# Kernel tuning notes

Measured on AMD Instinct MI355X. Metric: run time of the kernel, lower is better.

## Reference

```python
import jax, jax.numpy as jnp
import numpy as np

KERNEL_SIZE = 2
TEMPERATURE = 1.0
EPS = 1e-5


def _ln(y, g, b):
    mu = jnp.mean(y, axis=-1, keepdims=True)
    var = jnp.mean((y - mu) ** 2, axis=-1, keepdims=True)
    return g * (y - mu) * jax.lax.rsqrt(var + EPS) + b


def _window_sum_before(h, k):
    # sum of h shifted right by 1..k (zero padded), matching get_hidden_states_before
    B, L, H = h.shape
    out = jnp.zeros_like(h)
    for s in range(1, k + 1):
        out = out + jnp.pad(h, ((0, 0), (s, 0), (0, 0)))[:, :L, :]
    return out


def _window_sum_after(h, k):
    B, L, H = h.shape
    out = jnp.zeros_like(h)
    for s in range(1, k + 1):
        out = out + jnp.pad(h, ((0, 0), (0, s), (0, 0)))[:, s:, :]
    return out


def setup_inputs():
    H, B, L = 512, 8, 1024
    std = 0.1
    key = jax.random.key(0)
    ks = jax.random.split(key, 12)
    return {
        "word_inputs": jax.random.normal(ks[0], (B, L, H), jnp.float32),
        "mask": jnp.zeros((B, L), jnp.float32),  # 1 = padding
        "num_layers": 3,
        "Wg": std * jax.random.normal(ks[1], (4 * H, 8 * H), jnp.float32),
        "bg": std * jax.random.normal(ks[2], (8 * H,), jnp.float32),
        "Wemb": std * jax.random.normal(ks[3], (H, 8 * H), jnp.float32),
        "Wdg": std * jax.random.normal(ks[4], (2 * H, 2 * H), jnp.float32),
        "bdg": std * jax.random.normal(ks[5], (2 * H,), jnp.float32),
        "Wdf": std * jax.random.normal(ks[6], (2 * H, H), jnp.float32),
        "bdf": std * jax.random.normal(ks[7], (H,), jnp.float32),
        "Wet": std * jax.random.normal(ks[8], (H, H), jnp.float32),
        "bet": jnp.zeros((H,), jnp.float32),
        "W1": std * jax.random.normal(ks[9], (H, 2 * H), jnp.float32),
        "b1": jnp.zeros((2 * H,), jnp.float32),
        "W2": std * jax.random.normal(ks[10], (2 * H, H), jnp.float32),
        "b2": jnp.zeros((H,), jnp.float32),
        "ln_g": jnp.ones((11, H), jnp.float32),   # order: i,o,l,f1,f2,f3,f4,gd,go,gf,h
        "ln_b": jnp.zeros((11, H), jnp.float32),
    }


def reference(word_inputs, mask, num_layers, Wg, bg, Wemb, Wdg, bdg, Wdf, bdf,
              Wet, bet, W1, b1, W2, b2, ln_g, ln_b):
    B, L, H = word_inputs.shape
    seq_mask = (1.0 - mask)[:, :, None]          # (B,L,1), 1 = real token
    softmax_neg = (-mask * 1e25)[:, :, None]     # (B,L,1)
    lens = jnp.sum(seq_mask, axis=1)             # (B,1)

    x = word_inputs * seq_mask
    h, c = x, x
    dh = jnp.sum(h, axis=1) / lens               # (B,H) dummy/sentence node
    dc = jnp.sum(c, axis=1) / lens

    we_cat = x @ Wemb                            # (B,L,8H) embedding gate terms
    emb_tr = jnp.tanh(x @ Wet + bet)             # (B,L,H)

    # dummy-gate weight chunks, mirroring torch chunk/split layout
    gWxd, gWhd = Wdg[:H, :H], Wdg[H:, :H]
    gWxo, gWho = Wdg[:H, H:], Wdg[H:, H:]
    gbd, gbo = bdg[:H], bdg[H:]
    gWxf, gWhf = Wdf[:H], Wdf[H:]

    for _ in range(num_layers):
        hb = _window_sum_before(h, KERNEL_SIZE) * seq_mask
        ha = _window_sum_after(h, KERNEL_SIZE) * seq_mask
        cb = _window_sum_before(c, KERNEL_SIZE) * seq_mask
        ca = _window_sum_after(c, KERNEL_SIZE) * seq_mask
        d_in = jnp.broadcast_to(dh[:, None, :], (B, L, H))

        # single fused 4H -> 8H gate GEMM plus precomputed embedding gates
        gates = jnp.concatenate([h, hb, ha, d_in], axis=-1) @ Wg + bg + we_cat
        fl, fr, fc_, fd, gi, ge, gw, go = jnp.split(gates, 8, axis=-1)

        g_fl = jax.nn.sigmoid(_ln(fl, ln_g[3], ln_b[3]))
        g_fr = jax.nn.sigmoid(_ln(fr, ln_g[4], ln_b[4]))
        g_fc = jax.nn.sigmoid(_ln(fc_, ln_g[5], ln_b[5]))
        g_fd = jax.nn.sigmoid(_ln(fd, ln_g[6], ln_b[6]))
        g_i = jax.nn.sigmoid(_ln(gi, ln_g[0], ln_b[0]))
        g_e = jax.nn.sigmoid(_ln(ge, ln_g[2], ln_b[2]))
        g_o = jax.nn.sigmoid(_ln(go, ln_g[1], ln_b[1]))
        cand = jnp.tanh(gw)

        # normalize the five write sources across gates (S-LSTM softmax combination)
        five = jax.nn.softmax(
            jnp.stack([g_fl, g_fr, g_fc, g_fd, g_i], axis=0) / TEMPERATURE, axis=0)
        c_new = (five[0] * cb + five[1] * ca + five[2] * c
                 + five[3] * dc[:, None, :] + five[4] * cand)
        h_new = g_o * jnp.tanh(c_new) + g_e * emb_tr

        h = h_new * seq_mask
        c = c_new * seq_mask

        # dummy (sentence-level) node update with position softmax attention
        avg_h = jnp.sum(h, axis=1) / lens
        g_d = jax.nn.sigmoid(_ln(dh @ gWxd + avg_h @ gWhd + gbd, ln_g[7], ln_b[7]))
        g_do = jax.nn.sigmoid(_ln(dh @ gWxo + avg_h @ gWho + gbo, ln_g[8], ln_b[8]))
        g_f = jax.nn.sigmoid(_ln((dh @ gWxf)[:, None, :] + h @ gWhf + bdf,
                                 ln_g[9], ln_b[9]))          # (B,L,H)
        scores = jax.nn.softmax(
            jnp.concatenate([g_f + softmax_neg, g_d[:, None, :]], axis=1)
            / TEMPERATURE, axis=1)                            # (B,L+1,H)
        dc = jnp.sum(scores[:, :L] * c, axis=1) + scores[:, L] * dc
        dh = g_do * jnp.tanh(dc)

    # position-wise FFN + residual + final LayerNorm (dropout off / eval mode)
    out = h + (jnp.maximum(h @ W1 + b1, 0.0) @ W2 + b2)
    out = _ln(out, ln_g[10], ln_b[10])
    return out * seq_mask
```

## Files before the change

### kernel.cpp

```cpp
#include <hip/hip_runtime.h>
#include <hip/hip_bf16.h>

typedef __hip_bfloat16 bf16;
typedef __attribute__((ext_vector_type(8))) short bf16x8;
typedef __attribute__((ext_vector_type(4))) float f32x4;

#define B_ 8
#define L_ 1024
#define H_ 512
#define BL_ (B_ * L_)
#define BLH_ ((size_t)BL_ * H_)
#define NCH 32
#define CHL (L_ / NCH)
#define NLAYERS 3

__device__ __forceinline__ float b2f(bf16 x) { return __bfloat162float(x); }
__device__ __forceinline__ bf16  f2b(float x) { return __float2bfloat16(x); }
__device__ __forceinline__ short f2bs(float x) { bf16 h = f2b(x); return *(short*)&h; }
__device__ __forceinline__ float bsf(short s) {
    union { unsigned int i; float f; } u; u.i = ((unsigned int)(unsigned short)s) << 16; return u.f;
}
__device__ __forceinline__ float sigm(float x) { return 1.f / (1.f + expf(-x)); }

__device__ __forceinline__ void gload16(const void* g, void* l) {
    __builtin_amdgcn_global_load_lds((const __attribute__((address_space(1))) void*)g,
                                     (__attribute__((address_space(3))) void*)l, 16, 0, 0);
}


__global__ __launch_bounds__(256) void cvtT_k(const float* __restrict__ src, bf16* __restrict__ dst,
                                              int R, int C, int ldD, int co) {
    __shared__ float t[32][33];
    int tx = threadIdx.x & 31, ty = threadIdx.x >> 5;
    int c = blockIdx.x * 32 + tx;
    int rb = blockIdx.y * 32;
    #pragma unroll
    for (int i = 0; i < 4; ++i)
        t[ty + i * 8][tx] = src[(size_t)(rb + ty + i * 8) * C + c];
    __syncthreads();
    #pragma unroll
    for (int i = 0; i < 4; ++i)
        dst[(size_t)(blockIdx.x * 32 + ty + i * 8) * ldD + co + rb + tx] = f2b(t[tx][ty + i * 8]);
}

__global__ __launch_bounds__(256) void init_k(const float* __restrict__ word, const float* __restrict__ mask,
                                              bf16* __restrict__ xbf, bf16* __restrict__ h0, bf16* __restrict__ c0,
                                              bf16* __restrict__ A) {
    size_t idx = (size_t)blockIdx.x * 256 + threadIdx.x;
    if (idx >= BLH_) return;
    int bl = (int)(idx >> 9);
    int hh = (int)(idx & 511);
    float sm = 1.f - mask[bl];
    bf16 w = f2b(word[idx] * sm);
    xbf[idx] = w; h0[idx] = w; c0[idx] = w;
    A[((size_t)bl << 11) + 1536 + hh] = w;
}

__global__ __launch_bounds__(256) void lens_k(const float* __restrict__ mask, float* __restrict__ lens) {
    __shared__ float sr[4];
    int b = blockIdx.x, t = threadIdx.x;
    float s = 0.f;
    for (int l = t; l < L_; l += 256) s += 1.f - mask[b * L_ + l];
    #pragma unroll
    for (int off = 32; off > 0; off >>= 1) s += __shfl_down(s, off);
    if ((t & 63) == 0) sr[t >> 6] = s;
    __syncthreads();
    if (t == 0) lens[b] = sr[0] + sr[1] + sr[2] + sr[3];
}

__global__ __launch_bounds__(512) void colsum_k(const bf16* __restrict__ src, float* __restrict__ partial) {
    int h = threadIdx.x, ch = blockIdx.x, b = blockIdx.y;
    float s = 0.f;
    #pragma unroll 4
    for (int i = 0; i < CHL; ++i)
        s += b2f(src[((size_t)(b * L_ + ch * CHL + i) << 9) + h]);
    partial[((size_t)(b * NCH + ch) << 9) + h] = s;
}

__global__ __launch_bounds__(512) void avgcomb_k(const float* __restrict__ partial, const float* __restrict__ lens,
                                                 float* __restrict__ o1, float* __restrict__ o2) {
    int h = threadIdx.x, b = blockIdx.x;
    float s = 0.f;
    #pragma unroll
    for (int ch = 0; ch < NCH; ++ch) s += partial[((size_t)(b * NCH + ch) << 9) + h];
    float a = s / lens[b];
    o1[(b << 9) + h] = a;
    if (o2) o2[(b << 9) + h] = a;
}


__global__ __launch_bounds__(256) void gemm_mfma_k(const bf16* __restrict__ A, const bf16* __restrict__ Bt,
                                                   const float* __restrict__ bias, const float* __restrict__ addB,
                                                   bf16* __restrict__ C, int M, int N, int K, int mode) {
    __shared__ __align__(16) bf16 As[2 * 128 * 32];
    __shared__ __align__(16) bf16 Bs[2 * 128 * 32];
    const int tid = threadIdx.x;
    const int lane = tid & 63, wv = tid >> 6;
    const int wm = wv >> 1, wn = wv & 1;
    const int m0 = blockIdx.y * 128, n0 = blockIdx.x * 128;

    const int r0 = tid >> 2, c0 = (tid & 3) * 8;
    const bf16* Ar0 = A + (size_t)(m0 + r0) * K + c0;
    const bf16* Ar1 = A + (size_t)(m0 + r0 + 64) * K + c0;
    const bf16* Br0 = Bt + (size_t)(n0 + r0) * K + c0;
    const bf16* Br1 = Bt + (size_t)(n0 + r0 + 64) * K + c0;
    bf16* lA0 = As + (size_t)tid * 8;
    bf16* lA1 = As + (size_t)(tid + 256) * 8;
    bf16* lB0 = Bs + (size_t)tid * 8;
    bf16* lB1 = Bs + (size_t)(tid + 256) * 8;

    f32x4 acc[4][4] = {};
    const int fr = lane & 15, fq = lane >> 4;
    const bf16* aP = As + (size_t)(wm * 64 + fr) * 32 + fq * 8;
    const bf16* bP = Bs + (size_t)(wn * 64 + fr) * 32 + fq * 8;

    for (int k0 = 0; k0 < K; k0 += 64) {
        #pragma unroll
        for (int h = 0; h < 2; ++h) {
            gload16(Ar0 + k0 + h * 32, lA0 + h * 4096);
            gload16(Ar1 + k0 + h * 32, lA1 + h * 4096);
            gload16(Br0 + k0 + h * 32, lB0 + h * 4096);
            gload16(Br1 + k0 + h * 32, lB1 + h * 4096);
        }
        __syncthreads();
        #pragma unroll
        for (int h = 0; h < 2; ++h) {
            bf16x8 af[4], bfr[4];
            #pragma unroll
            for (int i = 0; i < 4; ++i) {
                af[i]  = *(const bf16x8*)(aP + h * 4096 + (size_t)i * 16 * 32);
                bfr[i] = *(const bf16x8*)(bP + h * 4096 + (size_t)i * 16 * 32);
            }
            #pragma unroll
            for (int i = 0; i < 4; ++i)
                #pragma unroll
                for (int j = 0; j < 4; ++j)
                    acc[i][j] = __builtin_amdgcn_mfma_f32_16x16x32_bf16(af[i], bfr[j], acc[i][j], 0, 0, 0);
        }
        __syncthreads();
    }
    const float* abp = addB ? addB + (size_t)(m0 >> 10) * N : nullptr;
    #pragma unroll
    for (int j = 0; j < 4; ++j) {
        int n = n0 + wn * 64 + j * 16 + fr;
        float bb = bias ? bias[n] : 0.f;
        if (abp) bb += abp[n];
        #pragma unroll
        for (int i = 0; i < 4; ++i) {
            #pragma unroll
            for (int r = 0; r < 4; ++r) {
                int m = m0 + wm * 64 + i * 16 + fq * 4 + r;
                float v = acc[i][j][r] + bb;
                if (mode == 1) v = fmaxf(v, 0.f);
                else if (mode == 2) v = tanhf(v);
                C[(size_t)m * N + n] = f2b(v);
            }
        }
    }
}


#define PRE_BUILD_BLOCKS ((int)(BLH_ / 8 / 256))
__global__ __launch_bounds__(256) void pre_k(const bf16* __restrict__ h, const float* __restrict__ mask,
                                             bf16* __restrict__ A, const float* __restrict__ dh,
                                             const bf16* __restrict__ WdhT, const float* __restrict__ bg,
                                             float* __restrict__ dhG) {
    __shared__ float a[512];
    if (blockIdx.x >= PRE_BUILD_BLOCKS) {
        int e = blockIdx.x - PRE_BUILD_BLOCKS;
        int b = e >> 4, nb = e & 15;
        int t = threadIdx.x;
        a[t] = dh[(b << 9) + t];
        a[t + 256] = dh[(b << 9) + t + 256];
        __syncthreads();
        int n = nb * 256 + t;
        const bf16* wr = WdhT + (size_t)n * 512;
        float acc = bg[n];
        #pragma unroll 8
        for (int i = 0; i < 64; ++i) {
            bf16x8 w = *(const bf16x8*)(wr + i * 8);
            #pragma unroll
            for (int j = 0; j < 8; ++j) acc = fmaf(a[i * 8 + j], bsf(w[j]), acc);
        }
        dhG[(size_t)b * 4096 + n] = acc;
        return;
    }
    int i = blockIdx.x * 256 + threadIdx.x;
    int h8 = i & 63, bl = i >> 6;
    int l = bl & 1023;
    float sm = 1.f - mask[bl];
    size_t src = ((size_t)bl << 9) + (h8 << 3);
    bf16x8 hv = *(const bf16x8*)(h + src);
    float hb[8] = {}, ha[8] = {};
    if (l >= 1) { bf16x8 v = *(const bf16x8*)(h + src - 512);
        #pragma unroll
        for (int e = 0; e < 8; ++e) hb[e] += bsf(v[e]); }
    if (l >= 2) { bf16x8 v = *(const bf16x8*)(h + src - 1024);
        #pragma unroll
        for (int e = 0; e < 8; ++e) hb[e] += bsf(v[e]); }
    if (l <= L_ - 2) { bf16x8 v = *(const bf16x8*)(h + src + 512);
        #pragma unroll
        for (int e = 0; e < 8; ++e) ha[e] += bsf(v[e]); }
    if (l <= L_ - 3) { bf16x8 v = *(const bf16x8*)(h + src + 1024);
        #pragma unroll
        for (int e = 0; e < 8; ++e) ha[e] += bsf(v[e]); }
    bf16x8 hbv, hav;
    #pragma unroll
    for (int e = 0; e < 8; ++e) { hbv[e] = f2bs(hb[e] * sm); hav[e] = f2bs(ha[e] * sm); }
    size_t base = ((size_t)bl << 11) + (h8 << 3);
    *(bf16x8*)(A + base)        = hv;
    *(bf16x8*)(A + base + 512)  = hbv;
    *(bf16x8*)(A + base + 1024) = hav;
}

__global__ __launch_bounds__(256) void fuse_k(const bf16* __restrict__ gates,
                                              const float* __restrict__ lng, const float* __restrict__ lnb,
                                              const bf16* __restrict__ cin, const bf16* __restrict__ emb,
                                              const float* __restrict__ mask, const float* __restrict__ dc,
                                              bf16* __restrict__ hout, bf16* __restrict__ cout) {
    const int lane = threadIdx.x & 63;
    const int bl = (blockIdx.x << 2) + (threadIdx.x >> 6);
    const int l = bl & 1023, b = bl >> 10;
    const float sm = 1.f - mask[bl];
    const int e0 = lane << 3;
    const bf16* gp = gates + ((size_t)bl << 12) + e0;
    float g[8][8];
    #pragma unroll
    for (int j = 0; j < 8; ++j) {
        bf16x8 v = *(const bf16x8*)(gp + (j << 9));
        #pragma unroll
        for (int i = 0; i < 8; ++i) g[j][i] = bsf(v[i]);
    }
    const int js[7]  = {0, 1, 2, 3, 4, 5, 7};
    const int lis[7] = {3, 4, 5, 6, 0, 2, 1};
    #pragma unroll
    for (int jj = 0; jj < 7; ++jj) {
        const int j = js[jj];
        float s = 0.f, q = 0.f;
        #pragma unroll
        for (int i = 0; i < 8; ++i) { s += g[j][i]; q += g[j][i] * g[j][i]; }
        #pragma unroll
        for (int off = 32; off > 0; off >>= 1) { s += __shfl_xor(s, off); q += __shfl_xor(q, off); }
        float mu = s * (1.f / 512.f);
        float rs = rsqrtf(q * (1.f / 512.f) - mu * mu + 1e-5f);
        float gmv[8], btv[8];
        const float* gm = lng + lis[jj] * 512 + e0;
        const float* bt = lnb + lis[jj] * 512 + e0;
        *(float4*)&gmv[0] = *(const float4*)gm;       *(float4*)&gmv[4] = *(const float4*)(gm + 4);
        *(float4*)&btv[0] = *(const float4*)bt;       *(float4*)&btv[4] = *(const float4*)(bt + 4);
        #pragma unroll
        for (int i = 0; i < 8; ++i)
            g[j][i] = sigm(gmv[i] * (g[j][i] - mu) * rs + btv[i]);
    }
    size_t ci = ((size_t)bl << 9) + e0;
    float cm[8] = {}, cp[8] = {}, ccv[8], ev[8], dcv[8];
    {
        bf16x8 v = *(const bf16x8*)(cin + ci);
        #pragma unroll
        for (int i = 0; i < 8; ++i) ccv[i] = bsf(v[i]);
    }
    if (l >= 1) { bf16x8 v = *(const bf16x8*)(cin + ci - 512);
        #pragma unroll
        for (int i = 0; i < 8; ++i) cm[i] += bsf(v[i]); }
    if (l >= 2) { bf16x8 v = *(const bf16x8*)(cin + ci - 1024);
        #pragma unroll
        for (int i = 0; i < 8; ++i) cm[i] += bsf(v[i]); }
    if (l <= L_ - 2) { bf16x8 v = *(const bf16x8*)(cin + ci + 512);
        #pragma unroll
        for (int i = 0; i < 8; ++i) cp[i] += bsf(v[i]); }
    if (l <= L_ - 3) { bf16x8 v = *(const bf16x8*)(cin + ci + 1024);
        #pragma unroll
        for (int i = 0; i < 8; ++i) cp[i] += bsf(v[i]); }
    {
        bf16x8 v = *(const bf16x8*)(emb + ci);
        #pragma unroll
        for (int i = 0; i < 8; ++i) ev[i] = bsf(v[i]);
    }
    *(float4*)&dcv[0] = *(const float4*)(dc + (b << 9) + e0);
    *(float4*)&dcv[4] = *(const float4*)(dc + (b << 9) + e0 + 4);
    bf16x8 hv, cv;
    #pragma unroll
    for (int i = 0; i < 8; ++i) {
        float mx = fmaxf(fmaxf(fmaxf(g[0][i], g[1][i]), fmaxf(g[2][i], g[3][i])), g[4][i]);
        float w0 = expf(g[0][i] - mx), w1 = expf(g[1][i] - mx), w2 = expf(g[2][i] - mx);
        float w3 = expf(g[3][i] - mx), w4 = expf(g[4][i] - mx);
        float inv = 1.f / (w0 + w1 + w2 + w3 + w4);
        float cand = tanhf(g[6][i]);
        float cn = (w0 * cm[i] * sm + w1 * cp[i] * sm + w2 * ccv[i] + w3 * dcv[i] + w4 * cand) * inv;
        float hn = g[7][i] * tanhf(cn) + g[5][i] * ev[i];
        hv[i] = f2bs(hn * sm);
        cv[i] = f2bs(cn * sm);
    }
    *(bf16x8*)(hout + ci) = hv;
    *(bf16x8*)(cout + ci) = cv;
}

__global__ __launch_bounds__(512) void dgu_k(const float* __restrict__ dh, const float* __restrict__ partial,
                                             const float* __restrict__ lens,
                                             const bf16* __restrict__ WdgT, const float* __restrict__ bdg,
                                             const bf16* __restrict__ WdfT0, const float* __restrict__ bdf,
                                             const float* __restrict__ lng, const float* __restrict__ lnb,
                                             float* __restrict__ gd, float* __restrict__ gdo, float* __restrict__ u) {
    __shared__ float a2[1024];
    __shared__ float sred[16];
    int t = threadIdx.x, bx = blockIdx.x, b = blockIdx.y;
    a2[t] = dh[(b << 9) + t];
    {
        float s = 0.f;
        #pragma unroll
        for (int ch = 0; ch < NCH; ++ch) s += partial[((size_t)(b * NCH + ch) << 9) + t];
        a2[512 + t] = s / lens[b];
    }
    __syncthreads();
    if (bx == 2) {
        const bf16* wr = WdfT0 + (size_t)t * 512;
        float acc = bdf[t];
        #pragma unroll 8
        for (int i = 0; i < 64; ++i) {
            bf16x8 w = *(const bf16x8*)(wr + i * 8);
            #pragma unroll
            for (int j = 0; j < 8; ++j) acc = fmaf(a2[i * 8 + j], bsf(w[j]), acc);
        }
        u[(b << 9) + t] = acc;
        return;
    }
    int col = (bx << 9) + t;
    const bf16* wr = WdgT + (size_t)col * 1024;
    float acc = bdg[col];
    #pragma unroll 8
    for (int i = 0; i < 128; ++i) {
        bf16x8 w = *(const bf16x8*)(wr + i * 8);
        #pragma unroll
        for (int j = 0; j < 8; ++j) acc = fmaf(a2[i * 8 + j], bsf(w[j]), acc);
    }
    float s = acc, q = acc * acc;
    #pragma unroll
    for (int off = 32; off > 0; off >>= 1) { s += __shfl_down(s, off); q += __shfl_down(q, off); }
    int w = t >> 6;
    if ((t & 63) == 0) { sred[w] = s; sred[8 + w] = q; }
    __syncthreads();
    float S = 0.f, Q = 0.f;
    #pragma unroll
    for (int i = 0; i < 8; ++i) { S += sred[i]; Q += sred[8 + i]; }
    float mu = S * (1.f / 512.f);
    float var = Q * (1.f / 512.f) - mu * mu;
    int li = 7 + bx;
    float n = lng[li * 512 + t] * (acc - mu) * rsqrtf(var + 1e-5f) + lnb[li * 512 + t];
    float g = sigm(n);
    if (bx) gdo[(b << 9) + t] = g; else gd[(b << 9) + t] = g;
}

__global__ __launch_bounds__(256) void gfln_k(bf16* __restrict__ gf, const float* __restrict__ lng,
                                              const float* __restrict__ lnb) {
    const int lane = threadIdx.x & 63;
    const int bl = (blockIdx.x << 2) + (threadIdx.x >> 6);
    const int e0 = lane << 3;
    size_t ci = ((size_t)bl << 9) + e0;
    float v[8];
    {
        bf16x8 gv = *(const bf16x8*)(gf + ci);
        #pragma unroll
        for (int i = 0; i < 8; ++i) v[i] = bsf(gv[i]);
    }
    float s = 0.f, q = 0.f;
    #pragma unroll
    for (int i = 0; i < 8; ++i) { s += v[i]; q += v[i] * v[i]; }
    #pragma unroll
    for (int off = 32; off > 0; off >>= 1) { s += __shfl_xor(s, off); q += __shfl_xor(q, off); }
    float mu = s * (1.f / 512.f);
    float rs = rsqrtf(q * (1.f / 512.f) - mu * mu + 1e-5f);
    float gmv[8], btv[8];
    const float* gm = lng + 9 * 512 + e0;
    const float* bt = lnb + 9 * 512 + e0;
    *(float4*)&gmv[0] = *(const float4*)gm;  *(float4*)&gmv[4] = *(const float4*)(gm + 4);
    *(float4*)&btv[0] = *(const float4*)bt;  *(float4*)&btv[4] = *(const float4*)(bt + 4);
    bf16x8 ov;
    #pragma unroll
    for (int i = 0; i < 8; ++i) ov[i] = f2bs(sigm(gmv[i] * (v[i] - mu) * rs + btv[i]));
    *(bf16x8*)(gf + ci) = ov;
}

__global__ __launch_bounds__(512) void attnp_k(const bf16* __restrict__ gf, const float* __restrict__ mask,
                                               const bf16* __restrict__ cc, float* __restrict__ pm,
                                               float* __restrict__ ps, float* __restrict__ pa) {
    int h = threadIdx.x, ch = blockIdx.x, b = blockIdx.y;
    float m = -INFINITY, s = 0.f, acc = 0.f;
    for (int i = 0; i < CHL; ++i) {
        int l = ch * CHL + i;
        size_t idx = ((size_t)(b * L_ + l) << 9) + h;
        float v = b2f(gf[idx]) - mask[b * L_ + l] * 1e25f;
        float mn = fmaxf(m, v);
        float sc = expf(m - mn);
        float p = expf(v - mn);
        s = s * sc + p;
        acc = acc * sc + p * b2f(cc[idx]);
        m = mn;
    }
    size_t o = ((size_t)(b * NCH + ch) << 9) + h;
    pm[o] = m; ps[o] = s; pa[o] = acc;
}

__global__ __launch_bounds__(512) void attnc_k(const float* __restrict__ pm, const float* __restrict__ ps,
                                               const float* __restrict__ pa, const float* __restrict__ gd,
                                               const float* __restrict__ gdo, float* __restrict__ dc,
                                               float* __restrict__ dh) {
    int h = threadIdx.x, b = blockIdx.x;
    float M = -INFINITY, S = 0.f, A = 0.f;
    #pragma unroll
    for (int ch = 0; ch < NCH; ++ch) {
        size_t o = ((size_t)(b * NCH + ch) << 9) + h;
        float m = pm[o], s = ps[o], a = pa[o];
        float Mn = fmaxf(M, m);
        float e1 = expf(M - Mn), e2 = expf(m - Mn);
        S = S * e1 + s * e2;
        A = A * e1 + a * e2;
        M = Mn;
    }
    float v = gd[(b << 9) + h];
    float Mn = fmaxf(M, v);
    float e1 = expf(M - Mn), e2 = expf(v - Mn);
    float dcold = dc[(b << 9) + h];
    S = S * e1 + e2;
    A = A * e1 + e2 * dcold;
    float dcn = A / S;
    dc[(b << 9) + h] = dcn;
    dh[(b << 9) + h] = gdo[(b << 9) + h] * tanhf(dcn);
}

__global__ __launch_bounds__(256) void final_k(const bf16* __restrict__ hfin, const bf16* __restrict__ t2,
                                               const float* __restrict__ lng, const float* __restrict__ lnb,
                                               const float* __restrict__ mask, float* __restrict__ out) {
    const int lane = threadIdx.x & 63;
    const int bl = (blockIdx.x << 2) + (threadIdx.x >> 6);
    const int e0 = lane << 3;
    size_t ci = ((size_t)bl << 9) + e0;
    float v[8];
    {
        bf16x8 a = *(const bf16x8*)(hfin + ci);
        bf16x8 bb = *(const bf16x8*)(t2 + ci);
        #pragma unroll
        for (int i = 0; i < 8; ++i) v[i] = bsf(a[i]) + bsf(bb[i]);
    }
    float s = 0.f, q = 0.f;
    #pragma unroll
    for (int i = 0; i < 8; ++i) { s += v[i]; q += v[i] * v[i]; }
    #pragma unroll
    for (int off = 32; off > 0; off >>= 1) { s += __shfl_xor(s, off); q += __shfl_xor(q, off); }
    float mu = s * (1.f / 512.f);
    float rs = rsqrtf(q * (1.f / 512.f) - mu * mu + 1e-5f);
    float gmv[8], btv[8];
    const float* gm = lng + 10 * 512 + e0;
    const float* bt = lnb + 10 * 512 + e0;
    *(float4*)&gmv[0] = *(const float4*)gm;  *(float4*)&gmv[4] = *(const float4*)(gm + 4);
    *(float4*)&btv[0] = *(const float4*)bt;  *(float4*)&btv[4] = *(const float4*)(bt + 4);
    float sm = 1.f - mask[bl];
    float o[8];
    #pragma unroll
    for (int i = 0; i < 8; ++i) o[i] = (gmv[i] * (v[i] - mu) * rs + btv[i]) * sm;
    *(float4*)(out + ci)     = *(float4*)&o[0];
    *(float4*)(out + ci + 4) = *(float4*)&o[4];
}


extern "C" void kernel_launch(void* const* d_in, const int* in_sizes, int n_in,
                              void* d_out, int out_size, void* d_ws, size_t ws_size,
                              hipStream_t stream) {
    const float* word = (const float*)d_in[0];
    const float* mask = (const float*)d_in[1];
    const float* Wg   = (const float*)d_in[3];
    const float* bg   = (const float*)d_in[4];
    const float* Wemb = (const float*)d_in[5];
    const float* Wdg  = (const float*)d_in[6];
    const float* bdg  = (const float*)d_in[7];
    const float* Wdf  = (const float*)d_in[8];
    const float* bdf  = (const float*)d_in[9];
    const float* Wet  = (const float*)d_in[10];
    const float* bet  = (const float*)d_in[11];
    const float* W1   = (const float*)d_in[12];
    const float* b1   = (const float*)d_in[13];
    const float* W2   = (const float*)d_in[14];
    const float* b2   = (const float*)d_in[15];
    const float* lng  = (const float*)d_in[16];
    const float* lnb  = (const float*)d_in[17];
    float* out = (float*)d_out;

    char* base = (char*)d_ws;
    size_t off = 0;
    auto alloc = [&](size_t bytes) -> void* {
        void* r = base + off;
        off += (bytes + 255) & ~(size_t)255;
        return r;
    };
    bf16* h0    = (bf16*)alloc(BLH_ * 2);
    bf16* h1    = (bf16*)alloc(BLH_ * 2);
    bf16* c0    = (bf16*)alloc(BLH_ * 2);
    bf16* c1    = (bf16*)alloc(BLH_ * 2);
    bf16* xbf   = (bf16*)alloc(BLH_ * 2);
    bf16* emb   = (bf16*)alloc(BLH_ * 2);
    bf16* Abuf  = (bf16*)alloc((size_t)BL_ * 2048 * 2);
    bf16* gf    = (bf16*)alloc(BLH_ * 2);
    bf16* t1    = (bf16*)alloc((size_t)BL_ * 1024 * 2);
    bf16* t2    = (bf16*)alloc(BLH_ * 2);
    bf16* WcatT = (bf16*)alloc((size_t)4096 * 2048 * 2);
    bf16* gates = (bf16*)alloc((size_t)BL_ * 4096 * 2);
    bf16* WetT  = (bf16*)alloc((size_t)512 * 512 * 2);
    bf16* WhfT  = (bf16*)alloc((size_t)512 * 512 * 2);
    bf16* W1T   = (bf16*)alloc((size_t)1024 * 512 * 2);
    bf16* W2T   = (bf16*)alloc((size_t)512 * 1024 * 2);
    bf16* WdhT  = (bf16*)alloc((size_t)4096 * 512 * 2);
    bf16* WdgT  = (bf16*)alloc((size_t)1024 * 1024 * 2);
    bf16* WdfT0 = (bf16*)alloc((size_t)512 * 512 * 2);
    float* dhG  = (float*)alloc((size_t)B_ * 4096 * 4);
    float* pm   = (float*)alloc((size_t)B_ * NCH * H_ * 4);
    float* ps   = (float*)alloc((size_t)B_ * NCH * H_ * 4);
    float* pa   = (float*)alloc((size_t)B_ * NCH * H_ * 4);
    float* lens = (float*)alloc(B_ * 4);
    float* dh   = (float*)alloc(B_ * H_ * 4);
    float* dc   = (float*)alloc(B_ * H_ * 4);
    float* avgh = (float*)alloc(B_ * H_ * 4);
    float* gd   = (float*)alloc(B_ * H_ * 4);
    float* gdo  = (float*)alloc(B_ * H_ * 4);
    float* u    = (float*)alloc(B_ * H_ * 4);
    (void)ws_size; (void)in_sizes; (void)n_in; (void)out_size; (void)avgh;

    cvtT_k<<<dim3(128, 48), 256, 0, stream>>>(Wg,   WcatT, 1536, 4096, 2048, 0);
    cvtT_k<<<dim3(128, 16), 256, 0, stream>>>(Wemb, WcatT,  512, 4096, 2048, 1536);
    cvtT_k<<<dim3(16, 16),  256, 0, stream>>>(Wet,  WetT,   512,  512,  512, 0);
    cvtT_k<<<dim3(16, 16),  256, 0, stream>>>(Wdf + (size_t)512 * 512, WhfT, 512, 512, 512, 0);
    cvtT_k<<<dim3(32, 16),  256, 0, stream>>>(W1,   W1T,    512, 1024,  512, 0);
    cvtT_k<<<dim3(16, 32),  256, 0, stream>>>(W2,   W2T,   1024,  512, 1024, 0);
    cvtT_k<<<dim3(128, 16), 256, 0, stream>>>(Wg + (size_t)1536 * 4096, WdhT, 512, 4096, 512, 0);
    cvtT_k<<<dim3(32, 32),  256, 0, stream>>>(Wdg,  WdgT,  1024, 1024, 1024, 0);
    cvtT_k<<<dim3(16, 16),  256, 0, stream>>>(Wdf,  WdfT0,  512,  512,  512, 0);

    const int eb = (int)((BLH_ + 255) / 256);
    init_k<<<eb, 256, 0, stream>>>(word, mask, xbf, h0, c0, Abuf);
    lens_k<<<B_, 256, 0, stream>>>(mask, lens);
    colsum_k<<<dim3(NCH, B_), 512, 0, stream>>>(xbf, pm);
    avgcomb_k<<<B_, 512, 0, stream>>>(pm, lens, dh, dc);

    gemm_mfma_k<<<dim3(4, 64), 256, 0, stream>>>(xbf, WetT, bet, nullptr, emb, BL_, 512, 512, 2);

    bf16 *hcur = h0, *ccur = c0, *hnxt = h1, *cnxt = c1;
    for (int layer = 0; layer < NLAYERS; ++layer) {
        pre_k<<<PRE_BUILD_BLOCKS + 16 * B_, 256, 0, stream>>>(hcur, mask, Abuf, dh, WdhT, bg, dhG);
        gemm_mfma_k<<<dim3(32, 64), 256, 0, stream>>>(Abuf, WcatT, nullptr, dhG, gates, BL_, 4096, 2048, 0);
        fuse_k<<<BL_ / 4, 256, 0, stream>>>(gates, lng, lnb, ccur, emb, mask, dc, hnxt, cnxt);
        colsum_k<<<dim3(NCH, B_), 512, 0, stream>>>(hnxt, pm);
        dgu_k<<<dim3(3, B_), 512, 0, stream>>>(dh, pm, lens, WdgT, bdg, WdfT0, bdf, lng, lnb, gd, gdo, u);
        gemm_mfma_k<<<dim3(4, 64), 256, 0, stream>>>(hnxt, WhfT, nullptr, u, gf, BL_, 512, 512, 0);
        gfln_k<<<BL_ / 4, 256, 0, stream>>>(gf, lng, lnb);
        attnp_k<<<dim3(NCH, B_), 512, 0, stream>>>(gf, mask, cnxt, pm, ps, pa);
        attnc_k<<<B_, 512, 0, stream>>>(pm, ps, pa, gd, gdo, dc, dh);
        bf16* t;
        t = hcur; hcur = hnxt; hnxt = t;
        t = ccur; ccur = cnxt; cnxt = t;
    }

    gemm_mfma_k<<<dim3(8, 64), 256, 0, stream>>>(hcur, W1T, b1, nullptr, t1, BL_, 1024, 512, 1);
    gemm_mfma_k<<<dim3(4, 64), 256, 0, stream>>>(t1, W2T, b2, nullptr, t2, BL_, 512, 1024, 0);
    final_k<<<BL_ / 4, 256, 0, stream>>>(hcur, t2, lng, lnb, mask, out);
}
```

Before: 1.265 ms.

## Skip final-layer dummy-node update, fuse prep launches, fold attention combine into pre_k

Unrolls the three-layer loop on the host and drops the last layer's sentence-node update (colsum, dgu, gf GEMM, gfln, attention partials). The final output depends only on h, so that work is dead. Merges the nine weight-transpose launches, the init kernel and the lens kernel into one prep_k dispatch indexed by block id. Folds the attention-combine step into the dh-GEMV blocks of the next layer's pre_k, with ping-pong dc buffers. The aim is to cut launch count and redundant work, at the cost of each pre_k dh block recomputing the combine redundantly.

```diff
diff --git a/kernel.cpp b/kernel.cpp
--- a/kernel.cpp
+++ b/kernel.cpp
@@ -28,44 +28,75 @@
 }
 
 
-__global__ __launch_bounds__(256) void cvtT_k(const float* __restrict__ src, bf16* __restrict__ dst,
-                                              int R, int C, int ldD, int co) {
-    __shared__ float t[32][33];
-    int tx = threadIdx.x & 31, ty = threadIdx.x >> 5;
-    int c = blockIdx.x * 32 + tx;
-    int rb = blockIdx.y * 32;
+__device__ __forceinline__ void cvtT_body(const float* __restrict__ src, bf16* __restrict__ dst,
+                                          int C, int ldD, int co, int bx, int by, int tid,
+                                          float (*t)[33]) {
+    int tx = tid & 31, ty = tid >> 5;
+    int c = bx * 32 + tx;
+    int rb = by * 32;
     #pragma unroll
     for (int i = 0; i < 4; ++i)
         t[ty + i * 8][tx] = src[(size_t)(rb + ty + i * 8) * C + c];
     __syncthreads();
     #pragma unroll
     for (int i = 0; i < 4; ++i)
-        dst[(size_t)(blockIdx.x * 32 + ty + i * 8) * ldD + co + rb + tx] = f2b(t[tx][ty + i * 8]);
-}
-
-__global__ __launch_bounds__(256) void init_k(const float* __restrict__ word, const float* __restrict__ mask,
-                                              bf16* __restrict__ xbf, bf16* __restrict__ h0, bf16* __restrict__ c0,
+        dst[(size_t)(bx * 32 + ty + i * 8) * ldD + co + rb + tx] = f2b(t[tx][ty + i * 8]);
+}
+
+#define J0 6144
+#define J1 (J0 + 2048)
+#define J2 (J1 + 256)
+#define J3 (J2 + 256)
+#define J4 (J3 + 512)
+#define J5 (J4 + 512)
+#define J6 (J5 + 2048)
+#define J7 (J6 + 1024)
+#define J8 (J7 + 256)
+#define JL (J8 + 8)
+#define JI (JL + 16384)
+
+__global__ __launch_bounds__(256) void prep_k(const float* __restrict__ Wg, const float* __restrict__ Wemb,
+                                              const float* __restrict__ Wet, const float* __restrict__ Wdf,
+                                              const float* __restrict__ W1, const float* __restrict__ W2,
+                                              const float* __restrict__ Wdg, const float* __restrict__ mask,
+                                              const float* __restrict__ word,
+                                              bf16* __restrict__ WcatT, bf16* __restrict__ WetT,
+                                              bf16* __restrict__ WhfT, bf16* __restrict__ W1T,
+                                              bf16* __restrict__ W2T, bf16* __restrict__ WdhT,
+                                              bf16* __restrict__ WdgT, bf16* __restrict__ WdfT0,
+                                              float* __restrict__ lens, bf16* __restrict__ xbf,
+                                              bf16* __restrict__ h0, bf16* __restrict__ c0,
                                               bf16* __restrict__ A) {
-    size_t idx = (size_t)blockIdx.x * 256 + threadIdx.x;
-    if (idx >= BLH_) return;
+    __shared__ float t[32][33];
+    const int bid = blockIdx.x, tid = threadIdx.x;
+    if (bid < J0) { cvtT_body(Wg, WcatT, 4096, 2048, 0, bid & 127, bid >> 7, tid, t); return; }
+    if (bid < J1) { int b = bid - J0; cvtT_body(Wemb, WcatT, 4096, 2048, 1536, b & 127, b >> 7, tid, t); return; }
+    if (bid < J2) { int b = bid - J1; cvtT_body(Wet, WetT, 512, 512, 0, b & 15, b >> 4, tid, t); return; }
+    if (bid < J3) { int b = bid - J2; cvtT_body(Wdf + (size_t)512 * 512, WhfT, 512, 512, 0, b & 15, b >> 4, tid, t); return; }
+    if (bid < J4) { int b = bid - J3; cvtT_body(W1, W1T, 1024, 512, 0, b & 31, b >> 5, tid, t); return; }
+    if (bid < J5) { int b = bid - J4; cvtT_body(W2, W2T, 512, 1024, 0, b & 15, b >> 4, tid, t); return; }
+    if (bid < J6) { int b = bid - J5; cvtT_body(Wg + (size_t)1536 * 4096, WdhT, 4096, 512, 0, b & 127, b >> 7, tid, t); return; }
+    if (bid < J7) { int b = bid - J6; cvtT_body(Wdg, WdgT, 1024, 1024, 0, b & 31, b >> 5, tid, t); return; }
+    if (bid < J8) { int b = bid - J7; cvtT_body(Wdf, WdfT0, 512, 512, 0, b & 15, b >> 4, tid, t); return; }
+    if (bid < JL) {
+        int b = bid - J8;
+        float s = 0.f;
+        for (int l = tid; l < L_; l += 256) s += 1.f - mask[b * L_ + l];
+        #pragma unroll
+        for (int off = 32; off > 0; off >>= 1) s += __shfl_down(s, off);
+        float* sr = (float*)t;
+        if ((tid & 63) == 0) sr[tid >> 6] = s;
+        __syncthreads();
+        if (tid == 0) lens[b] = sr[0] + sr[1] + sr[2] + sr[3];
+        return;
+    }
+    size_t idx = (size_t)(bid - JL) * 256 + tid;
     int bl = (int)(idx >> 9);
     int hh = (int)(idx & 511);
     float sm = 1.f - mask[bl];
     bf16 w = f2b(word[idx] * sm);
     xbf[idx] = w; h0[idx] = w; c0[idx] = w;
     A[((size_t)bl << 11) + 1536 + hh] = w;
-}
-
-__global__ __launch_bounds__(256) void lens_k(const float* __restrict__ mask, float* __restrict__ lens) {
-    __shared__ float sr[4];
-    int b = blockIdx.x, t = threadIdx.x;
-    float s = 0.f;
-    for (int l = t; l < L_; l += 256) s += 1.f - mask[b * L_ + l];
-    #pragma unroll
-    for (int off = 32; off > 0; off >>= 1) s += __shfl_down(s, off);
-    if ((t & 63) == 0) sr[t >> 6] = s;
-    __syncthreads();
-    if (t == 0) lens[b] = sr[0] + sr[1] + sr[2] + sr[3];
 }
 
 __global__ __launch_bounds__(512) void colsum_k(const bf16* __restrict__ src, float* __restrict__ partial) {
@@ -85,7 +116,7 @@
     for (int ch = 0; ch < NCH; ++ch) s += partial[((size_t)(b * NCH + ch) << 9) + h];
     float a = s / lens[b];
     o1[(b << 9) + h] = a;
-    if (o2) o2[(b << 9) + h] = a;
+    o2[(b << 9) + h] = a;
 }
 
 
@@ -162,18 +193,48 @@
 
 #define PRE_BUILD_BLOCKS ((int)(BLH_ / 8 / 256))
 __global__ __launch_bounds__(256) void pre_k(const bf16* __restrict__ h, const float* __restrict__ mask,
-                                             bf16* __restrict__ A, const float* __restrict__ dh,
+                                             bf16* __restrict__ A, float* __restrict__ dh,
                                              const bf16* __restrict__ WdhT, const float* __restrict__ bg,
-                                             float* __restrict__ dhG) {
+                                             float* __restrict__ dhG,
+                                             const float* __restrict__ pm, const float* __restrict__ ps,
+                                             const float* __restrict__ pa, const float* __restrict__ gd,
+                                             const float* __restrict__ gdo, const float* __restrict__ dcIn,
+                                             float* __restrict__ dcOut, int useAttn) {
     __shared__ float a[512];
     if (blockIdx.x >= PRE_BUILD_BLOCKS) {
         int e = blockIdx.x - PRE_BUILD_BLOCKS;
         int b = e >> 4, nb = e & 15;
         int t = threadIdx.x;
-        a[t] = dh[(b << 9) + t];
-        a[t + 256] = dh[(b << 9) + t + 256];
+        if (!useAttn) {
+            a[t] = dh[(b << 9) + t];
+            a[t + 256] = dh[(b << 9) + t + 256];
+        } else {
+            for (int hh = t; hh < 512; hh += 256) {
+                float M = -INFINITY, S = 0.f, Acc = 0.f;
+                #pragma unroll
+                for (int ch = 0; ch < NCH; ++ch) {
+                    size_t o = ((size_t)(b * NCH + ch) << 9) + hh;
+                    float m = pm[o], s = ps[o], aa = pa[o];
+                    float Mn = fmaxf(M, m);
+                    float e1 = expf(M - Mn), e2 = expf(m - Mn);
+                    S = S * e1 + s * e2;
+                    Acc = Acc * e1 + aa * e2;
+                    M = Mn;
+                }
+                float v = gd[(b << 9) + hh];
+                float Mn = fmaxf(M, v);
+                float e1 = expf(M - Mn), e2 = expf(v - Mn);
+                float dcold = dcIn[(b << 9) + hh];
+                S = S * e1 + e2;
+                Acc = Acc * e1 + e2 * dcold;
+                float dcn = Acc / S;
+                float dhv = gdo[(b << 9) + hh] * tanhf(dcn);
+                a[hh] = dhv;
+                if (nb == 0) { dcOut[(b << 9) + hh] = dcn; dh[(b << 9) + hh] = dhv; }
+            }
+        }
         __syncthreads();
-        int n = nb * 256 + t;
+        int n = nb * 256 + threadIdx.x;
         const bf16* wr = WdhT + (size_t)n * 512;
         float acc = bg[n];
         #pragma unroll 8
@@ -398,33 +459,6 @@
     }
     size_t o = ((size_t)(b * NCH + ch) << 9) + h;
     pm[o] = m; ps[o] = s; pa[o] = acc;
-}
-
-__global__ __launch_bounds__(512) void attnc_k(const float* __restrict__ pm, const float* __restrict__ ps,
-                                               const float* __restrict__ pa, const float* __restrict__ gd,
-                                               const float* __restrict__ gdo, float* __restrict__ dc,
-                                               float* __restrict__ dh) {
-    int h = threadIdx.x, b = blockIdx.x;
-    float M = -INFINITY, S = 0.f, A = 0.f;
-    #pragma unroll
-    for (int ch = 0; ch < NCH; ++ch) {
-        size_t o = ((size_t)(b * NCH + ch) << 9) + h;
-        float m = pm[o], s = ps[o], a = pa[o];
-        float Mn = fmaxf(M, m);
-        float e1 = expf(M - Mn), e2 = expf(m - Mn);
-        S = S * e1 + s * e2;
-        A = A * e1 + a * e2;
-        M = Mn;
-    }
-    float v = gd[(b << 9) + h];
-    float Mn = fmaxf(M, v);
-    float e1 = expf(M - Mn), e2 = expf(v - Mn);
-    float dcold = dc[(b << 9) + h];
-    S = S * e1 + e2;
-    A = A * e1 + e2 * dcold;
-    float dcn = A / S;
-    dc[(b << 9) + h] = dcn;
-    dh[(b << 9) + h] = gdo[(b << 9) + h] * tanhf(dcn);
 }
 
 __global__ __launch_bounds__(256) void final_k(const bf16* __restrict__ hfin, const bf16* __restrict__ t2,
@@ -511,53 +545,55 @@
     bf16* WdgT  = (bf16*)alloc((size_t)1024 * 1024 * 2);
     bf16* WdfT0 = (bf16*)alloc((size_t)512 * 512 * 2);
     float* dhG  = (float*)alloc((size_t)B_ * 4096 * 4);
+    float* cs   = (float*)alloc((size_t)B_ * NCH * H_ * 4);
     float* pm   = (float*)alloc((size_t)B_ * NCH * H_ * 4);
     float* ps   = (float*)alloc((size_t)B_ * NCH * H_ * 4);
     float* pa   = (float*)alloc((size_t)B_ * NCH * H_ * 4);
     float* lens = (float*)alloc(B_ * 4);
     float* dh   = (float*)alloc(B_ * H_ * 4);
-    float* dc   = (float*)alloc(B_ * H_ * 4);
-    float* avgh = (float*)alloc(B_ * H_ * 4);
+    float* dcA  = (float*)alloc(B_ * H_ * 4);
+    float* dcB  = (float*)alloc(B_ * H_ * 4);
     float* gd   = (float*)alloc(B_ * H_ * 4);
     float* gdo  = (float*)alloc(B_ * H_ * 4);
     float* u    = (float*)alloc(B_ * H_ * 4);
-    (void)ws_size; (void)in_sizes; (void)n_in; (void)out_size; (void)avgh;
-
-    cvtT_k<<<dim3(128, 48), 256, 0, stream>>>(Wg,   WcatT, 1536, 4096, 2048, 0);
-    cvtT_k<<<dim3(128, 16), 256, 0, stream>>>(Wemb, WcatT,  512, 4096, 2048, 1536);
-    cvtT_k<<<dim3(16, 16),  256, 0, stream>>>(Wet,  WetT,   512,  512,  512, 0);
-    cvtT_k<<<dim3(16, 16),  256, 0, stream>>>(Wdf + (size_t)512 * 512, WhfT, 512, 512, 512, 0);
-    cvtT_k<<<dim3(32, 16),  256, 0, stream>>>(W1,   W1T,    512, 1024,  512, 0);
-    cvtT_k<<<dim3(16, 32),  256, 0, stream>>>(W2,   W2T,   1024,  512, 1024, 0);
-    cvtT_k<<<dim3(128, 16), 256, 0, stream>>>(Wg + (size_t)1536 * 4096, WdhT, 512, 4096, 512, 0);
-    cvtT_k<<<dim3(32, 32),  256, 0, stream>>>(Wdg,  WdgT,  1024, 1024, 1024, 0);
-    cvtT_k<<<dim3(16, 16),  256, 0, stream>>>(Wdf,  WdfT0,  512,  512,  512, 0);
-
-    const int eb = (int)((BLH_ + 255) / 256);
-    init_k<<<eb, 256, 0, stream>>>(word, mask, xbf, h0, c0, Abuf);
-    lens_k<<<B_, 256, 0, stream>>>(mask, lens);
-    colsum_k<<<dim3(NCH, B_), 512, 0, stream>>>(xbf, pm);
-    avgcomb_k<<<B_, 512, 0, stream>>>(pm, lens, dh, dc);
+    (void)ws_size; (void)in_sizes; (void)n_in; (void)out_size;
+
+    prep_k<<<JI, 256, 0, stream>>>(Wg, Wemb, Wet, Wdf, W1, W2, Wdg, mask, word,
+                                   WcatT, WetT, WhfT, W1T, W2T, WdhT, WdgT, WdfT0,
+                                   lens, xbf, h0, c0, Abuf);
+    colsum_k<<<dim3(NCH, B_), 512, 0, stream>>>(xbf, cs);
+    avgcomb_k<<<B_, 512, 0, stream>>>(cs, lens, dh, dcA);
 
     gemm_mfma_k<<<dim3(4, 64), 256, 0, stream>>>(xbf, WetT, bet, nullptr, emb, BL_, 512, 512, 2);
 
-    bf16 *hcur = h0, *ccur = c0, *hnxt = h1, *cnxt = c1;
-    for (int layer = 0; layer < NLAYERS; ++layer) {
-        pre_k<<<PRE_BUILD_BLOCKS + 16 * B_, 256, 0, stream>>>(hcur, mask, Abuf, dh, WdhT, bg, dhG);
-        gemm_mfma_k<<<dim3(32, 64), 256, 0, stream>>>(Abuf, WcatT, nullptr, dhG, gates, BL_, 4096, 2048, 0);
-        fuse_k<<<BL_ / 4, 256, 0, stream>>>(gates, lng, lnb, ccur, emb, mask, dc, hnxt, cnxt);
-        colsum_k<<<dim3(NCH, B_), 512, 0, stream>>>(hnxt, pm);
-        dgu_k<<<dim3(3, B_), 512, 0, stream>>>(dh, pm, lens, WdgT, bdg, WdfT0, bdf, lng, lnb, gd, gdo, u);
-        gemm_mfma_k<<<dim3(4, 64), 256, 0, stream>>>(hnxt, WhfT, nullptr, u, gf, BL_, 512, 512, 0);
-        gfln_k<<<BL_ / 4, 256, 0, stream>>>(gf, lng, lnb);
-        attnp_k<<<dim3(NCH, B_), 512, 0, stream>>>(gf, mask, cnxt, pm, ps, pa);
-        attnc_k<<<B_, 512, 0, stream>>>(pm, ps, pa, gd, gdo, dc, dh);
-        bf16* t;
-        t = hcur; hcur = hnxt; hnxt = t;
-        t = ccur; ccur = cnxt; cnxt = t;
-    }
-
-    gemm_mfma_k<<<dim3(8, 64), 256, 0, stream>>>(hcur, W1T, b1, nullptr, t1, BL_, 1024, 512, 1);
+    const int preg = PRE_BUILD_BLOCKS + 16 * B_;
+
+    pre_k<<<preg, 256, 0, stream>>>(h0, mask, Abuf, dh, WdhT, bg, dhG,
+                                    nullptr, nullptr, nullptr, nullptr, nullptr, nullptr, nullptr, 0);
+    gemm_mfma_k<<<dim3(32, 64), 256, 0, stream>>>(Abuf, WcatT, nullptr, dhG, gates, BL_, 4096, 2048, 0);
+    fuse_k<<<BL_ / 4, 256, 0, stream>>>(gates, lng, lnb, c0, emb, mask, dcA, h1, c1);
+    colsum_k<<<dim3(NCH, B_), 512, 0, stream>>>(h1, cs);
+    dgu_k<<<dim3(3, B_), 512, 0, stream>>>(dh, cs, lens, WdgT, bdg, WdfT0, bdf, lng, lnb, gd, gdo, u);
+    gemm_mfma_k<<<dim3(4, 64), 256, 0, stream>>>(h1, WhfT, nullptr, u, gf, BL_, 512, 512, 0);
+    gfln_k<<<BL_ / 4, 256, 0, stream>>>(gf, lng, lnb);
+    attnp_k<<<dim3(NCH, B_), 512, 0, stream>>>(gf, mask, c1, pm, ps, pa);
+
+    pre_k<<<preg, 256, 0, stream>>>(h1, mask, Abuf, dh, WdhT, bg, dhG,
+                                    pm, ps, pa, gd, gdo, dcA, dcB, 1);
+    gemm_mfma_k<<<dim3(32, 64), 256, 0, stream>>>(Abuf, WcatT, nullptr, dhG, gates, BL_, 4096, 2048, 0);
+    fuse_k<<<BL_ / 4, 256, 0, stream>>>(gates, lng, lnb, c1, emb, mask, dcB, h0, c0);
+    colsum_k<<<dim3(NCH, B_), 512, 0, stream>>>(h0, cs);
+    dgu_k<<<dim3(3, B_), 512, 0, stream>>>(dh, cs, lens, WdgT, bdg, WdfT0, bdf, lng, lnb, gd, gdo, u);
+    gemm_mfma_k<<<dim3(4, 64), 256, 0, stream>>>(h0, WhfT, nullptr, u, gf, BL_, 512, 512, 0);
+    gfln_k<<<BL_ / 4, 256, 0, stream>>>(gf, lng, lnb);
+    attnp_k<<<dim3(NCH, B_), 512, 0, stream>>>(gf, mask, c0, pm, ps, pa);
+
+    pre_k<<<preg, 256, 0, stream>>>(h0, mask, Abuf, dh, WdhT, bg, dhG,
+                                    pm, ps, pa, gd, gdo, dcB, dcA, 1);
+    gemm_mfma_k<<<dim3(32, 64), 256, 0, stream>>>(Abuf, WcatT, nullptr, dhG, gates, BL_, 4096, 2048, 0);
+    fuse_k<<<BL_ / 4, 256, 0, stream>>>(gates, lng, lnb, c0, emb, mask, dcA, h1, c1);
+
+    gemm_mfma_k<<<dim3(8, 64), 256, 0, stream>>>(h1, W1T, b1, nullptr, t1, BL_, 1024, 512, 1);
     gemm_mfma_k<<<dim3(4, 64), 256, 0, stream>>>(t1, W2T, b2, nullptr, t2, BL_, 512, 1024, 0);
-    final_k<<<BL_ / 4, 256, 0, stream>>>(hcur, t2, lng, lnb, mask, out);
-}
+    final_k<<<BL_ / 4, 256, 0, stream>>>(h1, t2, lng, lnb, mask, out);
+}
```

Result: faster. 1.183 ms (-6.4%).
